# Optimization experiments

Measured on AMD Instinct MI355X. Metric: run time of the kernel, lower is better.

## Reference

```python
import jax, jax.numpy as jnp
import numpy as np

N_NODES = 50000
N_EDGES = 800000
IN_FEATS = 128
H_FEATS = 64
NUM_CLASSES = 2
K = 3
LAMBDA_MAX = 2.0  # standard upper bound for normalized-Laplacian max eigenvalue


def setup_inputs() -> dict:
    key = jax.random.key(0)
    ks = jax.random.split(key, 16)
    s = 0.05
    return {
        "in_feat": jax.random.normal(ks[0], (N_NODES, IN_FEATS), jnp.float32),
        "src": jax.random.randint(ks[1], (N_EDGES,), 0, N_NODES, jnp.int32),
        "dst": jax.random.randint(ks[2], (N_EDGES,), 0, N_NODES, jnp.int32),
        "W1": jax.random.normal(ks[3], (H_FEATS, IN_FEATS), jnp.float32) * s,
        "b1": jnp.zeros((H_FEATS,), jnp.float32),
        "W2": jax.random.normal(ks[4], (H_FEATS, H_FEATS), jnp.float32) * s,
        "b2": jnp.zeros((H_FEATS,), jnp.float32),
        "Wc1": jax.random.normal(ks[5], (H_FEATS, K * H_FEATS), jnp.float32) * s,
        "bc1": jnp.zeros((H_FEATS,), jnp.float32),
        "Wc2": jax.random.normal(ks[6], (H_FEATS, K * H_FEATS), jnp.float32) * s,
        "bc2": jnp.zeros((H_FEATS,), jnp.float32),
        "W3": jax.random.normal(ks[7], (H_FEATS, H_FEATS), jnp.float32) * s,
        "b3": jnp.zeros((H_FEATS,), jnp.float32),
        "W4": jax.random.normal(ks[8], (NUM_CLASSES, H_FEATS), jnp.float32) * s,
        "b4": jnp.zeros((NUM_CLASSES,), jnp.float32),
    }


def _cheb_conv(h, src, dst, d_invsqrt, W, b, k):
    """DGL ChebConv: Chebyshev recursion on scaled normalized Laplacian,
    concat k terms along feature dim, then Linear + relu (default activation)."""
    n = h.shape[0]
    re_norm = 2.0 / LAMBDA_MAX

    def a_norm(x):  # D^{-1/2} A D^{-1/2} x via edge-list SpMM
        msg = (x * d_invsqrt)[src]                              # [E, F]
        agg = jax.ops.segment_sum(msg, dst, num_segments=n)     # [N, F]
        return agg * d_invsqrt

    X0 = h
    Xs = [X0]
    X1 = -re_norm * a_norm(X0) + X0 * (re_norm - 1.0)
    Xs.append(X1)
    for _ in range(2, k):
        Xi = -2.0 * re_norm * a_norm(X1) + X1 * (2.0 * (re_norm - 1.0)) - X0
        Xs.append(Xi)
        X0, X1 = X1, Xi
    Xt = jnp.concatenate(Xs, axis=1)                            # [N, k*F]
    return jax.nn.relu(Xt @ W.T + b)


def reference(in_feat, src, dst, W1, b1, W2, b2, Wc1, bc1, Wc2, bc2, W3, b3, W4, b4):
    n = in_feat.shape[0]
    # in-degrees from dst, clamp(min=1), D^{-1/2}
    deg = jax.ops.segment_sum(jnp.ones_like(dst, jnp.float32), dst, num_segments=n)
    d_invsqrt = jnp.power(jnp.maximum(deg, 1.0), -0.5)[:, None]  # [N, 1]

    h = jax.nn.relu(in_feat @ W1.T + b1)
    h = jax.nn.relu(h @ W2.T + b2)
    h = _cheb_conv(h, src, dst, d_invsqrt, Wc1, bc1, K)
    h = _cheb_conv(h, src, dst, d_invsqrt, Wc2, bc2, K)
    h = jax.nn.relu(h @ W3.T + b3)
    h = h @ W4.T + b4
    return h
```

## Files before the change

kernel.cpp:

```cpp
#include <hip/hip_runtime.h>
#include <hip/hip_fp16.h>
#include <math.h>

#define NN 50000
#define NE 800000
#define INF 128
#define H 64
#define ELLCAP 64
#define NB_G ((NN + 63) / 64)
#define WOFF_W1 0
#define WOFF_W2 8192
#define WOFF_WC1 12288
#define WOFF_WC2 24576
#define WOFF_W3 36864
#define WTOT 40960
#define NB_CVTW (WTOT / 2048)

#define PSHIFT 8
#define NPART2 196
#define CAP 8192
#define NB_BINA 128
#define EPB (NE / NB_BINA)
#define EPT_A 25

#define TSCALE 64.0f
#define TSCALE_INV 0.015625f

typedef _Float16 half8_t __attribute__((ext_vector_type(8)));
typedef float float4_t __attribute__((ext_vector_type(4)));
typedef float float2_t __attribute__((ext_vector_type(2)));

__device__ __forceinline__ half8_t load_cvt8(const float* p) {
  float4 a = *(const float4*)(p);
  float4 b = *(const float4*)(p + 4);
  half8_t h;
  h[0] = (_Float16)a.x; h[1] = (_Float16)a.y; h[2] = (_Float16)a.z; h[3] = (_Float16)a.w;
  h[4] = (_Float16)b.x; h[5] = (_Float16)b.y; h[6] = (_Float16)b.z; h[7] = (_Float16)b.w;
  return h;
}

__device__ __forceinline__ unsigned char enc1(float x) {
  return (unsigned char)(__builtin_amdgcn_cvt_pk_fp8_f32(x, x, 0u, false) & 0xFFu);
}
__device__ __forceinline__ unsigned int enc4(float a, float b, float c, float d) {
  unsigned int v = __builtin_amdgcn_cvt_pk_fp8_f32(a, b, 0u, false);
  v = __builtin_amdgcn_cvt_pk_fp8_f32(c, d, v, true);
  return v;
}
__device__ __forceinline__ void dec8(unsigned int lo, unsigned int hi, float* f) {
  float2_t a = __builtin_amdgcn_cvt_pk_f32_fp8(lo, false);
  float2_t b = __builtin_amdgcn_cvt_pk_f32_fp8(lo, true);
  float2_t c = __builtin_amdgcn_cvt_pk_f32_fp8(hi, false);
  float2_t d = __builtin_amdgcn_cvt_pk_f32_fp8(hi, true);
  f[0] = a[0]; f[1] = a[1]; f[2] = b[0]; f[3] = b[1];
  f[4] = c[0]; f[5] = c[1]; f[6] = d[0]; f[7] = d[1];
}
__device__ __forceinline__ void dec16(uint4 q, float* f) {
  dec8(q.x, q.y, f);
  dec8(q.z, q.w, f + 8);
}

__global__ __launch_bounds__(256) void k_binA(const int* __restrict__ src, const int* __restrict__ dst,
                                              int* __restrict__ gcount, int* __restrict__ bucket,
                                              const float* __restrict__ W1, const float* __restrict__ W2,
                                              const float* __restrict__ Wc1, const float* __restrict__ Wc2,
                                              const float* __restrict__ W3, _Float16* __restrict__ w16) {
  int b = blockIdx.x;
  if (b >= NB_BINA) {
    int i0 = (b - NB_BINA) * 2048 + threadIdx.x * 8;
#pragma unroll
    for (int k = 0; k < 8; ++k) {
      int id = i0 + k;
      if (id < WTOT) {
        float v;
        if (id < WOFF_W2) v = W1[id];
        else if (id < WOFF_WC1) v = W2[id - WOFF_W2];
        else if (id < WOFF_WC2) v = Wc1[id - WOFF_WC1];
        else if (id < WOFF_W3) v = Wc2[id - WOFF_WC2];
        else v = W3[id - WOFF_W3];
        w16[id] = (_Float16)v;
      }
    }
    return;
  }
  __shared__ int s_cnt[NPART2];
  __shared__ int s_base[NPART2];
  const int tid = threadIdx.x;
  if (tid < NPART2) s_cnt[tid] = 0;
  __syncthreads();
  const int e0 = b * EPB;
  int rec[EPT_A];
  int meta[EPT_A];
#pragma unroll
  for (int i = 0; i < EPT_A; ++i) {
    int off = i * 256 + tid;
    meta[i] = -1;
    if (off < EPB) {
      int e = e0 + off;
      int d = __builtin_nontemporal_load(&dst[e]);
      int s = __builtin_nontemporal_load(&src[e]);
      int p = d >> PSHIFT;
      rec[i] = s | ((d & 255) << 16);
      int slot = atomicAdd(&s_cnt[p], 1);
      meta[i] = (p << 13) | slot;
    }
  }
  __syncthreads();
  if (tid < NPART2) s_base[tid] = atomicAdd(&gcount[tid], s_cnt[tid]);
  __syncthreads();
#pragma unroll
  for (int i = 0; i < EPT_A; ++i) {
    if (meta[i] >= 0) {
      int p = meta[i] >> 13;
      int pos = s_base[p] + (meta[i] & 8191);
      if (pos < CAP) bucket[(size_t)p * CAP + pos] = rec[i];
    }
  }
}

__global__ __launch_bounds__(256) void k_binB(const int* __restrict__ gcount, const int* __restrict__ bucket,
                                              unsigned short* __restrict__ ell, int* __restrict__ cnt,
                                              float* __restrict__ dinv32) {
  __shared__ int s_cnt[256];
  const int tid = threadIdx.x;
  const int p = blockIdx.x;
  s_cnt[tid] = 0;
  __syncthreads();
  int n = gcount[p];
  n = n < CAP ? n : CAP;
  const int* bp = bucket + (size_t)p * CAP;
  int j = tid;
  for (; j + 3 * 256 < n; j += 4 * 256) {
    int r0 = bp[j], r1 = bp[j + 256], r2 = bp[j + 512], r3 = bp[j + 768];
    int c0 = atomicAdd(&s_cnt[r0 >> 16], 1);
    int c1 = atomicAdd(&s_cnt[r1 >> 16], 1);
    int c2 = atomicAdd(&s_cnt[r2 >> 16], 1);
    int c3 = atomicAdd(&s_cnt[r3 >> 16], 1);
    if (c0 < ELLCAP) ell[((size_t)((p << PSHIFT) + (r0 >> 16)) << 6) + c0] = (unsigned short)(r0 & 0xFFFF);
    if (c1 < ELLCAP) ell[((size_t)((p << PSHIFT) + (r1 >> 16)) << 6) + c1] = (unsigned short)(r1 & 0xFFFF);
    if (c2 < ELLCAP) ell[((size_t)((p << PSHIFT) + (r2 >> 16)) << 6) + c2] = (unsigned short)(r2 & 0xFFFF);
    if (c3 < ELLCAP) ell[((size_t)((p << PSHIFT) + (r3 >> 16)) << 6) + c3] = (unsigned short)(r3 & 0xFFFF);
  }
  for (; j < n; j += 256) {
    int r = bp[j];
    int dl = r >> 16;
    int c = atomicAdd(&s_cnt[dl], 1);
    if (c < ELLCAP) ell[((size_t)((p << PSHIFT) + dl) << 6) + c] = (unsigned short)(r & 0xFFFF);
  }
  __syncthreads();
  int node = (p << PSHIFT) + tid;
  if (node < NN) {
    int c = s_cnt[tid];
    cnt[node] = c;
    dinv32[node] = 1.0f / sqrtf((float)(c < 1 ? 1 : c));
  }
}

__global__ __launch_bounds__(256) void k_mlp(const float* __restrict__ in_feat,
                                             const _Float16* __restrict__ w16,
                                             const float* __restrict__ b1,
                                             const float* __restrict__ b2,
                                             const float* __restrict__ dinv32,
                                             _Float16* __restrict__ X0c,
                                             unsigned char* __restrict__ X0t, int N) {
  __shared__ _Float16 Hs[64][72];
  const int tid = threadIdx.x;
  const int wave = tid >> 6;
  const int lane = tid & 63;
  const int m = lane & 15;
  const int quad = lane >> 4;
  const int rbase = blockIdx.x * 64 + wave * 16;
  int arow = rbase + m;
  arow = arow < N ? arow : N - 1;
  const float* Ap = in_feat + (size_t)arow * INF + quad * 8;
  const _Float16* B1 = w16 + WOFF_W1 + (size_t)m * INF + quad * 8;
  float4_t acc[4] = {{0.f,0.f,0.f,0.f},{0.f,0.f,0.f,0.f},{0.f,0.f,0.f,0.f},{0.f,0.f,0.f,0.f}};
#pragma unroll
  for (int k0 = 0; k0 < INF; k0 += 32) {
    half8_t a = load_cvt8(Ap + k0);
    half8_t b0 = *(const half8_t*)(B1 + k0);
    half8_t b1f = *(const half8_t*)(B1 + 16 * INF + k0);
    half8_t b2f = *(const half8_t*)(B1 + 32 * INF + k0);
    half8_t b3f = *(const half8_t*)(B1 + 48 * INF + k0);
    acc[0] = __builtin_amdgcn_mfma_f32_16x16x32_f16(a, b0, acc[0], 0, 0, 0);
    acc[1] = __builtin_amdgcn_mfma_f32_16x16x32_f16(a, b1f, acc[1], 0, 0, 0);
    acc[2] = __builtin_amdgcn_mfma_f32_16x16x32_f16(a, b2f, acc[2], 0, 0, 0);
    acc[3] = __builtin_amdgcn_mfma_f32_16x16x32_f16(a, b3f, acc[3], 0, 0, 0);
  }
#pragma unroll
  for (int i = 0; i < 4; ++i)
#pragma unroll
    for (int t = 0; t < 4; ++t)
      Hs[wave * 16 + quad * 4 + i][t * 16 + m] = (_Float16)fmaxf(acc[t][i] + b1[t * 16 + m], 0.f);
  __syncthreads();
  const _Float16* Ap2 = &Hs[wave * 16 + m][quad * 8];
  const _Float16* B2 = w16 + WOFF_W2 + (size_t)m * H + quad * 8;
  float4_t acc2[4] = {{0.f,0.f,0.f,0.f},{0.f,0.f,0.f,0.f},{0.f,0.f,0.f,0.f},{0.f,0.f,0.f,0.f}};
#pragma unroll
  for (int k0 = 0; k0 < H; k0 += 32) {
    half8_t a = *(const half8_t*)(Ap2 + k0);
    half8_t b0 = *(const half8_t*)(B2 + k0);
    half8_t b1f = *(const half8_t*)(B2 + 16 * H + k0);
    half8_t b2f = *(const half8_t*)(B2 + 32 * H + k0);
    half8_t b3f = *(const half8_t*)(B2 + 48 * H + k0);
    acc2[0] = __builtin_amdgcn_mfma_f32_16x16x32_f16(a, b0, acc2[0], 0, 0, 0);
    acc2[1] = __builtin_amdgcn_mfma_f32_16x16x32_f16(a, b1f, acc2[1], 0, 0, 0);
    acc2[2] = __builtin_amdgcn_mfma_f32_16x16x32_f16(a, b2f, acc2[2], 0, 0, 0);
    acc2[3] = __builtin_amdgcn_mfma_f32_16x16x32_f16(a, b3f, acc2[3], 0, 0, 0);
  }
#pragma unroll
  for (int i = 0; i < 4; ++i) {
    int rr = rbase + quad * 4 + i;
    if (rr < N) {
      float dn = TSCALE * dinv32[rr];
#pragma unroll
      for (int t = 0; t < 4; ++t) {
        float v = fmaxf(acc2[t][i] + b2[t * 16 + m], 0.f);
        X0c[((size_t)rr << 6) + t * 16 + m] = (_Float16)v;
        X0t[((size_t)rr << 6) + t * 16 + m] = enc1(dn * v);
      }
    }
  }
}

__global__ __launch_bounds__(256) void k_spmm(const unsigned char* __restrict__ tabs,
                                              _Float16* __restrict__ outc,
                                              unsigned char* __restrict__ outt,
                                              const int* __restrict__ cnt,
                                              const float* __restrict__ dinv32,
                                              const unsigned short* __restrict__ ell, int N) {
  int wv = (blockIdx.x * 256 + threadIdx.x) >> 6;
  int lane = threadIdx.x & 63;
  int node = wv * 8 + (lane >> 3);
  if (node >= N) return;
  int c8 = (lane & 7) * 8;
  int deg0 = cnt[node];
  int deg = deg0 < ELLCAP ? deg0 : ELLCAP;
  const unsigned short* row = ell + ((size_t)node << 6);

  float acc[8] = {0.f, 0.f, 0.f, 0.f, 0.f, 0.f, 0.f, 0.f};
  float f[8];
  int j = 0;
  for (; j + 7 < deg; j += 8) {
    ushort4 ra = *(const ushort4*)(row + j);
    ushort4 rb = *(const ushort4*)(row + j + 4);
    uint2 q0 = *(const uint2*)(tabs + (((size_t)ra.x) << 6) + c8);
    uint2 q1 = *(const uint2*)(tabs + (((size_t)ra.y) << 6) + c8);
    uint2 q2 = *(const uint2*)(tabs + (((size_t)ra.z) << 6) + c8);
    uint2 q3 = *(const uint2*)(tabs + (((size_t)ra.w) << 6) + c8);
    uint2 q4 = *(const uint2*)(tabs + (((size_t)rb.x) << 6) + c8);
    uint2 q5 = *(const uint2*)(tabs + (((size_t)rb.y) << 6) + c8);
    uint2 q6 = *(const uint2*)(tabs + (((size_t)rb.z) << 6) + c8);
    uint2 q7 = *(const uint2*)(tabs + (((size_t)rb.w) << 6) + c8);
    dec8(q0.x, q0.y, f);
#pragma unroll
    for (int k = 0; k < 8; ++k) acc[k] += f[k];
    dec8(q1.x, q1.y, f);
#pragma unroll
    for (int k = 0; k < 8; ++k) acc[k] += f[k];
    dec8(q2.x, q2.y, f);
#pragma unroll
    for (int k = 0; k < 8; ++k) acc[k] += f[k];
    dec8(q3.x, q3.y, f);
#pragma unroll
    for (int k = 0; k < 8; ++k) acc[k] += f[k];
    dec8(q4.x, q4.y, f);
#pragma unroll
    for (int k = 0; k < 8; ++k) acc[k] += f[k];
    dec8(q5.x, q5.y, f);
#pragma unroll
    for (int k = 0; k < 8; ++k) acc[k] += f[k];
    dec8(q6.x, q6.y, f);
#pragma unroll
    for (int k = 0; k < 8; ++k) acc[k] += f[k];
    dec8(q7.x, q7.y, f);
#pragma unroll
    for (int k = 0; k < 8; ++k) acc[k] += f[k];
  }
  for (; j + 3 < deg; j += 4) {
    ushort4 ra = *(const ushort4*)(row + j);
    uint2 q0 = *(const uint2*)(tabs + (((size_t)ra.x) << 6) + c8);
    uint2 q1 = *(const uint2*)(tabs + (((size_t)ra.y) << 6) + c8);
    uint2 q2 = *(const uint2*)(tabs + (((size_t)ra.z) << 6) + c8);
    uint2 q3 = *(const uint2*)(tabs + (((size_t)ra.w) << 6) + c8);
    dec8(q0.x, q0.y, f);
#pragma unroll
    for (int k = 0; k < 8; ++k) acc[k] += f[k];
    dec8(q1.x, q1.y, f);
#pragma unroll
    for (int k = 0; k < 8; ++k) acc[k] += f[k];
    dec8(q2.x, q2.y, f);
#pragma unroll
    for (int k = 0; k < 8; ++k) acc[k] += f[k];
    dec8(q3.x, q3.y, f);
#pragma unroll
    for (int k = 0; k < 8; ++k) acc[k] += f[k];
  }
  for (; j < deg; ++j) {
    size_t s = row[j];
    uint2 q0 = *(const uint2*)(tabs + (s << 6) + c8);
    dec8(q0.x, q0.y, f);
#pragma unroll
    for (int k = 0; k < 8; ++k) acc[k] += f[k];
  }
  float dn = dinv32[node];
  float a = -dn * TSCALE_INV;
  float r[8];
#pragma unroll
  for (int k = 0; k < 8; ++k) r[k] = a * acc[k];
  half8_t ro;
#pragma unroll
  for (int k = 0; k < 8; ++k) ro[k] = (_Float16)r[k];
  *(half8_t*)(outc + ((size_t)node << 6) + c8) = ro;
  float sc = TSCALE * dn;
  uint2 q;
  q.x = enc4(sc * r[0], sc * r[1], sc * r[2], sc * r[3]);
  q.y = enc4(sc * r[4], sc * r[5], sc * r[6], sc * r[7]);
  *(uint2*)(outt + ((size_t)node << 6) + c8) = q;
}

__global__ __launch_bounds__(256) void k_gemmX2(const unsigned char* __restrict__ tabs,
                                                const _Float16* __restrict__ A0,
                                                const _Float16* __restrict__ A1,
                                                const _Float16* __restrict__ B,
                                                const float* __restrict__ bias,
                                                const float* __restrict__ dinv32,
                                                const int* __restrict__ cnt,
                                                const unsigned short* __restrict__ ell,
                                                _Float16* __restrict__ outc,
                                                unsigned char* __restrict__ outt, int N) {
  __shared__ _Float16 X2s[64][72];
  const int tid = threadIdx.x;
  const int wave = tid >> 6;
  const int lane = tid & 63;
  {
    int lrow = wave * 16 + (lane >> 2);
    int gnode = blockIdx.x * 64 + lrow;
    int gc = (lane & 3) * 16;
    float a16[16];
#pragma unroll
    for (int k = 0; k < 16; ++k) a16[k] = 0.f;
    int deg = 0;
    if (gnode < N) {
      int d0 = cnt[gnode];
      deg = d0 < ELLCAP ? d0 : ELLCAP;
    }
    const unsigned short* row = ell + ((size_t)gnode << 6);
    float f[16];
    int j = 0;
    for (; j + 3 < deg; j += 4) {
      ushort4 ra = *(const ushort4*)(row + j);
      uint4 q0 = *(const uint4*)(tabs + (((size_t)ra.x) << 6) + gc);
      uint4 q1 = *(const uint4*)(tabs + (((size_t)ra.y) << 6) + gc);
      uint4 q2 = *(const uint4*)(tabs + (((size_t)ra.z) << 6) + gc);
      uint4 q3 = *(const uint4*)(tabs + (((size_t)ra.w) << 6) + gc);
      dec16(q0, f);
#pragma unroll
      for (int k = 0; k < 16; ++k) a16[k] += f[k];
      dec16(q1, f);
#pragma unroll
      for (int k = 0; k < 16; ++k) a16[k] += f[k];
      dec16(q2, f);
#pragma unroll
      for (int k = 0; k < 16; ++k) a16[k] += f[k];
      dec16(q3, f);
#pragma unroll
      for (int k = 0; k < 16; ++k) a16[k] += f[k];
    }
    for (; j < deg; ++j) {
      size_t s = row[j];
      uint4 q0 = *(const uint4*)(tabs + (s << 6) + gc);
      dec16(q0, f);
#pragma unroll
      for (int k = 0; k < 16; ++k) a16[k] += f[k];
    }
    half8_t o0, o1;
    if (gnode < N) {
      float aa = -2.f * dinv32[gnode] * TSCALE_INV;
      half8_t x0a = *(const half8_t*)(A0 + ((size_t)gnode << 6) + gc);
      half8_t x0b = *(const half8_t*)(A0 + ((size_t)gnode << 6) + gc + 8);
#pragma unroll
      for (int k = 0; k < 8; ++k) {
        o0[k] = (_Float16)(aa * a16[k] - (float)x0a[k]);
        o1[k] = (_Float16)(aa * a16[k + 8] - (float)x0b[k]);
      }
    } else {
#pragma unroll
      for (int k = 0; k < 8; ++k) { o0[k] = (_Float16)0.f; o1[k] = (_Float16)0.f; }
    }
    *(half8_t*)(&X2s[lrow][gc]) = o0;
    *(half8_t*)(&X2s[lrow][gc + 8]) = o1;
  }
  __syncthreads();
  const int m = lane & 15;
  const int quad = lane >> 4;
  const int rbase = blockIdx.x * 64 + wave * 16;
  int arow = rbase + m;
  arow = arow < N ? arow : N - 1;
  const size_t ro = ((size_t)arow << 6) + quad * 8;
  const _Float16* Bp = B + (size_t)m * 192 + quad * 8;
  float4_t acc[4] = {{0.f,0.f,0.f,0.f},{0.f,0.f,0.f,0.f},{0.f,0.f,0.f,0.f},{0.f,0.f,0.f,0.f}};
#pragma unroll
  for (int k0 = 0; k0 < 192; k0 += 32) {
    half8_t a;
    if (k0 < 64) a = *(const half8_t*)(A0 + ro + k0);
    else if (k0 < 128) a = *(const half8_t*)(A1 + ro + (k0 - 64));
    else a = *(const half8_t*)(&X2s[wave * 16 + m][quad * 8 + (k0 - 128)]);
    half8_t b0 = *(const half8_t*)(Bp + k0);
    half8_t b1f = *(const half8_t*)(Bp + 16 * 192 + k0);
    half8_t b2f = *(const half8_t*)(Bp + 32 * 192 + k0);
    half8_t b3f = *(const half8_t*)(Bp + 48 * 192 + k0);
    acc[0] = __builtin_amdgcn_mfma_f32_16x16x32_f16(a, b0, acc[0], 0, 0, 0);
    acc[1] = __builtin_amdgcn_mfma_f32_16x16x32_f16(a, b1f, acc[1], 0, 0, 0);
    acc[2] = __builtin_amdgcn_mfma_f32_16x16x32_f16(a, b2f, acc[2], 0, 0, 0);
    acc[3] = __builtin_amdgcn_mfma_f32_16x16x32_f16(a, b3f, acc[3], 0, 0, 0);
  }
#pragma unroll
  for (int i = 0; i < 4; ++i) {
    int rr = rbase + quad * 4 + i;
    if (rr < N) {
      float dn = TSCALE * dinv32[rr];
#pragma unroll
      for (int t = 0; t < 4; ++t) {
        float v = fmaxf(acc[t][i] + bias[t * 16 + m], 0.f);
        outc[((size_t)rr << 6) + t * 16 + m] = (_Float16)v;
        outt[((size_t)rr << 6) + t * 16 + m] = enc1(dn * v);
      }
    }
  }
}

__global__ __launch_bounds__(256) void k_tail2(const unsigned char* __restrict__ tabs,
                                               const _Float16* __restrict__ A0,
                                               const _Float16* __restrict__ A1,
                                               const _Float16* __restrict__ w16,
                                               const float* __restrict__ bc2,
                                               const float* __restrict__ b3,
                                               const float* __restrict__ W4,
                                               const float* __restrict__ b4,
                                               const float* __restrict__ dinv32,
                                               const int* __restrict__ cnt,
                                               const unsigned short* __restrict__ ell,
                                               float* __restrict__ out, int N) {
  __shared__ _Float16 Y2s[64][72];
  __shared__ _Float16 Hs2[64][72];
  __shared__ float Hs3[64][65];
  const int tid = threadIdx.x;
  const int wave = tid >> 6;
  const int lane = tid & 63;
  {
    int lrow = wave * 16 + (lane >> 2);
    int gnode = blockIdx.x * 64 + lrow;
    int gc = (lane & 3) * 16;
    float a16[16];
#pragma unroll
    for (int k = 0; k < 16; ++k) a16[k] = 0.f;
    int deg = 0;
    if (gnode < N) {
      int d0 = cnt[gnode];
      deg = d0 < ELLCAP ? d0 : ELLCAP;
    }
    const unsigned short* row = ell + ((size_t)gnode << 6);
    float f[16];
    int j = 0;
    for (; j + 3 < deg; j += 4) {
      ushort4 ra = *(const ushort4*)(row + j);
      uint4 q0 = *(const uint4*)(tabs + (((size_t)ra.x) << 6) + gc);
      uint4 q1 = *(const uint4*)(tabs + (((size_t)ra.y) << 6) + gc);
      uint4 q2 = *(const uint4*)(tabs + (((size_t)ra.z) << 6) + gc);
      uint4 q3 = *(const uint4*)(tabs + (((size_t)ra.w) << 6) + gc);
      dec16(q0, f);
#pragma unroll
      for (int k = 0; k < 16; ++k) a16[k] += f[k];
      dec16(q1, f);
#pragma unroll
      for (int k = 0; k < 16; ++k) a16[k] += f[k];
      dec16(q2, f);
#pragma unroll
      for (int k = 0; k < 16; ++k) a16[k] += f[k];
      dec16(q3, f);
#pragma unroll
      for (int k = 0; k < 16; ++k) a16[k] += f[k];
    }
    for (; j < deg; ++j) {
      size_t s = row[j];
      uint4 q0 = *(const uint4*)(tabs + (s << 6) + gc);
      dec16(q0, f);
#pragma unroll
      for (int k = 0; k < 16; ++k) a16[k] += f[k];
    }
    half8_t o0, o1;
    if (gnode < N) {
      float aa = -2.f * dinv32[gnode] * TSCALE_INV;
      half8_t y0a = *(const half8_t*)(A0 + ((size_t)gnode << 6) + gc);
      half8_t y0b = *(const half8_t*)(A0 + ((size_t)gnode << 6) + gc + 8);
#pragma unroll
      for (int k = 0; k < 8; ++k) {
        o0[k] = (_Float16)(aa * a16[k] - (float)y0a[k]);
        o1[k] = (_Float16)(aa * a16[k + 8] - (float)y0b[k]);
      }
    } else {
#pragma unroll
      for (int k = 0; k < 8; ++k) { o0[k] = (_Float16)0.f; o1[k] = (_Float16)0.f; }
    }
    *(half8_t*)(&Y2s[lrow][gc]) = o0;
    *(half8_t*)(&Y2s[lrow][gc + 8]) = o1;
  }
  __syncthreads();
  const int m = lane & 15;
  const int quad = lane >> 4;
  const int rbase = blockIdx.x * 64 + wave * 16;
  int arow = rbase + m;
  arow = arow < N ? arow : N - 1;
  {
    const size_t ro = ((size_t)arow << 6) + quad * 8;
    const _Float16* Bp = w16 + WOFF_WC2 + (size_t)m * 192 + quad * 8;
    float4_t acc[4] = {{0.f,0.f,0.f,0.f},{0.f,0.f,0.f,0.f},{0.f,0.f,0.f,0.f},{0.f,0.f,0.f,0.f}};
#pragma unroll
    for (int k0 = 0; k0 < 192; k0 += 32) {
      half8_t a;
      if (k0 < 64) a = *(const half8_t*)(A0 + ro + k0);
      else if (k0 < 128) a = *(const half8_t*)(A1 + ro + (k0 - 64));
      else a = *(const half8_t*)(&Y2s[wave * 16 + m][quad * 8 + (k0 - 128)]);
      half8_t b0 = *(const half8_t*)(Bp + k0);
      half8_t b1f = *(const half8_t*)(Bp + 16 * 192 + k0);
      half8_t b2f = *(const half8_t*)(Bp + 32 * 192 + k0);
      half8_t b3f = *(const half8_t*)(Bp + 48 * 192 + k0);
      acc[0] = __builtin_amdgcn_mfma_f32_16x16x32_f16(a, b0, acc[0], 0, 0, 0);
      acc[1] = __builtin_amdgcn_mfma_f32_16x16x32_f16(a, b1f, acc[1], 0, 0, 0);
      acc[2] = __builtin_amdgcn_mfma_f32_16x16x32_f16(a, b2f, acc[2], 0, 0, 0);
      acc[3] = __builtin_amdgcn_mfma_f32_16x16x32_f16(a, b3f, acc[3], 0, 0, 0);
    }
#pragma unroll
    for (int i = 0; i < 4; ++i)
#pragma unroll
      for (int t = 0; t < 4; ++t)
        Hs2[wave * 16 + quad * 4 + i][t * 16 + m] =
            (_Float16)fmaxf(acc[t][i] + bc2[t * 16 + m], 0.f);
  }
  __syncthreads();
  {
    const _Float16* Ap = &Hs2[wave * 16 + m][quad * 8];
    const _Float16* Bp = w16 + WOFF_W3 + (size_t)m * H + quad * 8;
    float4_t acc[4] = {{0.f,0.f,0.f,0.f},{0.f,0.f,0.f,0.f},{0.f,0.f,0.f,0.f},{0.f,0.f,0.f,0.f}};
#pragma unroll
    for (int k0 = 0; k0 < H; k0 += 32) {
      half8_t a = *(const half8_t*)(Ap + k0);
      half8_t b0 = *(const half8_t*)(Bp + k0);
      half8_t b1f = *(const half8_t*)(Bp + 16 * H + k0);
      half8_t b2f = *(const half8_t*)(Bp + 32 * H + k0);
      half8_t b3f = *(const half8_t*)(Bp + 48 * H + k0);
      acc[0] = __builtin_amdgcn_mfma_f32_16x16x32_f16(a, b0, acc[0], 0, 0, 0);
      acc[1] = __builtin_amdgcn_mfma_f32_16x16x32_f16(a, b1f, acc[1], 0, 0, 0);
      acc[2] = __builtin_amdgcn_mfma_f32_16x16x32_f16(a, b2f, acc[2], 0, 0, 0);
      acc[3] = __builtin_amdgcn_mfma_f32_16x16x32_f16(a, b3f, acc[3], 0, 0, 0);
    }
#pragma unroll
    for (int i = 0; i < 4; ++i)
#pragma unroll
      for (int t = 0; t < 4; ++t)
        Hs3[wave * 16 + quad * 4 + i][t * 16 + m] = fmaxf(acc[t][i] + b3[t * 16 + m], 0.f);
  }
  __syncthreads();
  if (tid < 128) {
    int r = tid >> 1;
    int c = tid & 1;
    int row = blockIdx.x * 64 + r;
    if (row < N) {
      const float* w4 = W4 + c * 64;
      float s = 0.f;
#pragma unroll
      for (int k = 0; k < 64; ++k) s = fmaf(Hs3[r][k], w4[k], s);
      out[(size_t)row * 2 + c] = s + b4[c];
    }
  }
}

extern "C" void kernel_launch(void* const* d_in, const int* in_sizes, int n_in,
                              void* d_out, int out_size, void* d_ws, size_t ws_size,
                              hipStream_t stream) {
  const float* in_feat = (const float*)d_in[0];
  const int* src = (const int*)d_in[1];
  const int* dst = (const int*)d_in[2];
  const float* W1 = (const float*)d_in[3];
  const float* b1 = (const float*)d_in[4];
  const float* W2 = (const float*)d_in[5];
  const float* b2 = (const float*)d_in[6];
  const float* Wc1 = (const float*)d_in[7];
  const float* bc1 = (const float*)d_in[8];
  const float* Wc2 = (const float*)d_in[9];
  const float* bc2 = (const float*)d_in[10];
  const float* W3 = (const float*)d_in[11];
  const float* b3 = (const float*)d_in[12];
  const float* W4 = (const float*)d_in[13];
  const float* b4 = (const float*)d_in[14];
  float* out = (float*)d_out;

  char* ws = (char*)d_ws;
  size_t o = 0;
  auto carve = [&](size_t bytes) -> void* {
    o = (o + 255) & ~(size_t)255;
    void* p = ws + o;
    o += bytes;
    return p;
  };
  int* cnt = (int*)carve((size_t)NN * 4);
  unsigned short* ell = (unsigned short*)carve((size_t)NN * ELLCAP * 2);
  float* dinv32 = (float*)carve((size_t)NN * 4);
  _Float16* w16 = (_Float16*)carve((size_t)WTOT * 2);
  _Float16* X0c = (_Float16*)carve((size_t)NN * H * 2);
  unsigned char* X0t = (unsigned char*)carve((size_t)NN * H);
  _Float16* X1c = (_Float16*)carve((size_t)NN * H * 2);
  unsigned char* X1t = (unsigned char*)carve((size_t)NN * H);
  _Float16* Y0c = (_Float16*)carve((size_t)NN * H * 2);
  unsigned char* Y0t = (unsigned char*)carve((size_t)NN * H);
  _Float16* Y1c = (_Float16*)carve((size_t)NN * H * 2);
  unsigned char* Y1t = (unsigned char*)carve((size_t)NN * H);
  int* gcount = (int*)carve((size_t)NPART2 * 4);
  int* bucket = (int*)Y0c;
  (void)ws_size; (void)in_sizes; (void)n_in; (void)out_size;

  const int NB_S = (NN + 31) / 32;

  hipMemsetAsync(gcount, 0, (size_t)NPART2 * 4, stream);
  k_binA<<<NB_BINA + NB_CVTW, 256, 0, stream>>>(src, dst, gcount, bucket, W1, W2, Wc1, Wc2, W3, w16);
  k_binB<<<NPART2, 256, 0, stream>>>(gcount, bucket, ell, cnt, dinv32);
  k_mlp<<<NB_G, 256, 0, stream>>>(in_feat, w16, b1, b2, dinv32, X0c, X0t, NN);
  k_spmm<<<NB_S, 256, 0, stream>>>(X0t, X1c, X1t, cnt, dinv32, ell, NN);
  k_gemmX2<<<NB_G, 256, 0, stream>>>(X1t, X0c, X1c, w16 + WOFF_WC1, bc1, dinv32, cnt, ell, Y0c, Y0t, NN);
  k_spmm<<<NB_S, 256, 0, stream>>>(Y0t, Y1c, Y1t, cnt, dinv32, ell, NN);
  k_tail2<<<NB_G, 256, 0, stream>>>(Y1t, Y0c, Y1c, w16, bc2, b3, W4, b4, dinv32, cnt, ell, out, NN);
}
```

Baseline: 225.9 us.

## Sort nodes by degree within 64-node groups and stage ELL rows in LDS

k_binB now builds each partition's ELL rows in shared memory, then writes them to global memory as contiguous row copies instead of scattered 2-byte stores. It also computes a per-64-node counting sort by degree (perm8). The SpMM and fused gemm kernels use perm8 so that lanes in a wave handle nodes with similar degree, which is meant to reduce divergence in the neighbor loops. This costs an extra indirection load per node, about 35KB of extra LDS in binB, and full 128-byte row writes even for low-degree nodes.

```diff
diff --git a/kernel.cpp b/kernel.cpp
--- a/kernel.cpp
+++ b/kernel.cpp
@@ -18,6 +18,7 @@
 
 #define PSHIFT 8
 #define NPART2 196
+#define NPERM (NPART2 * 256)
 #define CAP 8192
 #define NB_BINA 128
 #define EPB (NE / NB_BINA)
@@ -120,11 +121,17 @@
 
 __global__ __launch_bounds__(256) void k_binB(const int* __restrict__ gcount, const int* __restrict__ bucket,
                                               unsigned short* __restrict__ ell, int* __restrict__ cnt,
-                                              float* __restrict__ dinv32) {
+                                              float* __restrict__ dinv32,
+                                              unsigned char* __restrict__ perm8) {
+  __shared__ unsigned short s_ell[256][68];
   __shared__ int s_cnt[256];
+  __shared__ int s_hist[4][65];
+  __shared__ int s_off[4][65];
+  __shared__ int s_base[4][65];
   const int tid = threadIdx.x;
   const int p = blockIdx.x;
   s_cnt[tid] = 0;
+  for (int i = tid; i < 4 * 65; i += 256) { ((int*)s_hist)[i] = 0; ((int*)s_off)[i] = 0; }
   __syncthreads();
   int n = gcount[p];
   n = n < CAP ? n : CAP;
@@ -136,23 +143,41 @@
     int c1 = atomicAdd(&s_cnt[r1 >> 16], 1);
     int c2 = atomicAdd(&s_cnt[r2 >> 16], 1);
     int c3 = atomicAdd(&s_cnt[r3 >> 16], 1);
-    if (c0 < ELLCAP) ell[((size_t)((p << PSHIFT) + (r0 >> 16)) << 6) + c0] = (unsigned short)(r0 & 0xFFFF);
-    if (c1 < ELLCAP) ell[((size_t)((p << PSHIFT) + (r1 >> 16)) << 6) + c1] = (unsigned short)(r1 & 0xFFFF);
-    if (c2 < ELLCAP) ell[((size_t)((p << PSHIFT) + (r2 >> 16)) << 6) + c2] = (unsigned short)(r2 & 0xFFFF);
-    if (c3 < ELLCAP) ell[((size_t)((p << PSHIFT) + (r3 >> 16)) << 6) + c3] = (unsigned short)(r3 & 0xFFFF);
+    if (c0 < ELLCAP) s_ell[r0 >> 16][c0] = (unsigned short)(r0 & 0xFFFF);
+    if (c1 < ELLCAP) s_ell[r1 >> 16][c1] = (unsigned short)(r1 & 0xFFFF);
+    if (c2 < ELLCAP) s_ell[r2 >> 16][c2] = (unsigned short)(r2 & 0xFFFF);
+    if (c3 < ELLCAP) s_ell[r3 >> 16][c3] = (unsigned short)(r3 & 0xFFFF);
   }
   for (; j < n; j += 256) {
     int r = bp[j];
     int dl = r >> 16;
     int c = atomicAdd(&s_cnt[dl], 1);
-    if (c < ELLCAP) ell[((size_t)((p << PSHIFT) + dl) << 6) + c] = (unsigned short)(r & 0xFFFF);
+    if (c < ELLCAP) s_ell[dl][c] = (unsigned short)(r & 0xFFFF);
   }
   __syncthreads();
   int node = (p << PSHIFT) + tid;
+  int deg = 0;
   if (node < NN) {
     int c = s_cnt[tid];
     cnt[node] = c;
     dinv32[node] = 1.0f / sqrtf((float)(c < 1 ? 1 : c));
+    deg = c < ELLCAP ? c : ELLCAP;
+  }
+  int g = tid >> 6;
+  atomicAdd(&s_hist[g][deg], 1);
+  __syncthreads();
+  if (tid < 4) {
+    int acc = 0;
+    for (int k = 0; k <= 64; ++k) { s_base[tid][k] = acc; acc += s_hist[tid][k]; }
+  }
+  __syncthreads();
+  int pos = s_base[g][deg] + atomicAdd(&s_off[g][deg], 1);
+  perm8[(size_t)(p << PSHIFT) + (g << 6) + pos] = (unsigned char)(tid & 63);
+  if (node < NN) {
+    const uint2* srcv = (const uint2*)&s_ell[tid][0];
+    uint2* dstv = (uint2*)(ell + ((size_t)node << 6));
+#pragma unroll
+    for (int k = 0; k < 16; ++k) dstv[k] = srcv[k];
   }
 }
 
@@ -228,10 +253,13 @@
                                               unsigned char* __restrict__ outt,
                                               const int* __restrict__ cnt,
                                               const float* __restrict__ dinv32,
-                                              const unsigned short* __restrict__ ell, int N) {
+                                              const unsigned short* __restrict__ ell,
+                                              const unsigned char* __restrict__ perm8, int N) {
   int wv = (blockIdx.x * 256 + threadIdx.x) >> 6;
   int lane = threadIdx.x & 63;
-  int node = wv * 8 + (lane >> 3);
+  int slot = wv * 8 + (lane >> 3);
+  if (slot >= NPERM) return;
+  int node = (slot & ~63) + perm8[slot];
   if (node >= N) return;
   int c8 = (lane & 7) * 8;
   int deg0 = cnt[node];
@@ -327,6 +355,7 @@
                                                 const float* __restrict__ dinv32,
                                                 const int* __restrict__ cnt,
                                                 const unsigned short* __restrict__ ell,
+                                                const unsigned char* __restrict__ perm8,
                                                 _Float16* __restrict__ outc,
                                                 unsigned char* __restrict__ outt, int N) {
   __shared__ _Float16 X2s[64][72];
@@ -334,7 +363,8 @@
   const int wave = tid >> 6;
   const int lane = tid & 63;
   {
-    int lrow = wave * 16 + (lane >> 2);
+    int lslot = wave * 16 + (lane >> 2);
+    int lrow = perm8[(size_t)blockIdx.x * 64 + lslot];
     int gnode = blockIdx.x * 64 + lrow;
     int gc = (lane & 3) * 16;
     float a16[16];
@@ -441,6 +471,7 @@
                                                const float* __restrict__ dinv32,
                                                const int* __restrict__ cnt,
                                                const unsigned short* __restrict__ ell,
+                                               const unsigned char* __restrict__ perm8,
                                                float* __restrict__ out, int N) {
   __shared__ _Float16 Y2s[64][72];
   __shared__ _Float16 Hs2[64][72];
@@ -449,7 +480,8 @@
   const int wave = tid >> 6;
   const int lane = tid & 63;
   {
-    int lrow = wave * 16 + (lane >> 2);
+    int lslot = wave * 16 + (lane >> 2);
+    int lrow = perm8[(size_t)blockIdx.x * 64 + lslot];
     int gnode = blockIdx.x * 64 + lrow;
     int gc = (lane & 3) * 16;
     float a16[16];
@@ -608,6 +640,7 @@
   unsigned short* ell = (unsigned short*)carve((size_t)NN * ELLCAP * 2);
   float* dinv32 = (float*)carve((size_t)NN * 4);
   _Float16* w16 = (_Float16*)carve((size_t)WTOT * 2);
+  unsigned char* perm8 = (unsigned char*)carve((size_t)NPERM);
   _Float16* X0c = (_Float16*)carve((size_t)NN * H * 2);
   unsigned char* X0t = (unsigned char*)carve((size_t)NN * H);
   _Float16* X1c = (_Float16*)carve((size_t)NN * H * 2);
@@ -620,14 +653,14 @@
   int* bucket = (int*)Y0c;
   (void)ws_size; (void)in_sizes; (void)n_in; (void)out_size;
 
-  const int NB_S = (NN + 31) / 32;
+  const int NB_S = NPERM / 32;
 
   hipMemsetAsync(gcount, 0, (size_t)NPART2 * 4, stream);
   k_binA<<<NB_BINA + NB_CVTW, 256, 0, stream>>>(src, dst, gcount, bucket, W1, W2, Wc1, Wc2, W3, w16);
-  k_binB<<<NPART2, 256, 0, stream>>>(gcount, bucket, ell, cnt, dinv32);
+  k_binB<<<NPART2, 256, 0, stream>>>(gcount, bucket, ell, cnt, dinv32, perm8);
   k_mlp<<<NB_G, 256, 0, stream>>>(in_feat, w16, b1, b2, dinv32, X0c, X0t, NN);
-  k_spmm<<<NB_S, 256, 0, stream>>>(X0t, X1c, X1t, cnt, dinv32, ell, NN);
-  k_gemmX2<<<NB_G, 256, 0, stream>>>(X1t, X0c, X1c, w16 + WOFF_WC1, bc1, dinv32, cnt, ell, Y0c, Y0t, NN);
-  k_spmm<<<NB_S, 256, 0, stream>>>(Y0t, Y1c, Y1t, cnt, dinv32, ell, NN);
-  k_tail2<<<NB_G, 256, 0, stream>>>(Y1t, Y0c, Y1c, w16, bc2, b3, W4, b4, dinv32, cnt, ell, out, NN);
-}
+  k_spmm<<<NB_S, 256, 0, stream>>>(X0t, X1c, X1t, cnt, dinv32, ell, perm8, NN);
+  k_gemmX2<<<NB_G, 256, 0, stream>>>(X1t, X0c, X1c, w16 + WOFF_WC1, bc1, dinv32, cnt, ell, perm8, Y0c, Y0t, NN);
+  k_spmm<<<NB_S, 256, 0, stream>>>(Y0t, Y1c, Y1t, cnt, dinv32, ell, perm8, NN);
+  k_tail2<<<NB_G, 256, 0, stream>>>(Y1t, Y0c, Y1c, w16, bc2, b3, W4, b4, dinv32, cnt, ell, perm8, out, NN);
+}
```

New measurement: 226.9 us. No clear change (+0.4%).

## Run MLP alongside edge binning and stage ELL rows in shared memory

Applied to the files above, without the earlier changes.

The first MLP blocks now run in the same launch as the edge-binning blocks, since the MLP no longer needs degree information. The fp8 degree-scaled copy of X0 is now produced in binB, after degrees are known, by re-reading the fp16 X0. binB builds ELL rows in shared memory and writes each node's row out as contiguous vector stores, replacing scattered 2-byte global stores. The counter memset is folded into the weight-conversion kernel. This costs an extra read of X0c and about 35KB of LDS per binB block.

```diff
diff --git a/kernel.cpp b/kernel.cpp
--- a/kernel.cpp
+++ b/kernel.cpp
@@ -60,67 +60,137 @@
   dec8(q.z, q.w, f + 8);
 }
 
-__global__ __launch_bounds__(256) void k_binA(const int* __restrict__ src, const int* __restrict__ dst,
-                                              int* __restrict__ gcount, int* __restrict__ bucket,
-                                              const float* __restrict__ W1, const float* __restrict__ W2,
-                                              const float* __restrict__ Wc1, const float* __restrict__ Wc2,
-                                              const float* __restrict__ W3, _Float16* __restrict__ w16) {
+__global__ __launch_bounds__(256) void k_pre(const float* __restrict__ W1, const float* __restrict__ W2,
+                                             const float* __restrict__ Wc1, const float* __restrict__ Wc2,
+                                             const float* __restrict__ W3, _Float16* __restrict__ w16,
+                                             int* __restrict__ gcount) {
   int b = blockIdx.x;
-  if (b >= NB_BINA) {
-    int i0 = (b - NB_BINA) * 2048 + threadIdx.x * 8;
-#pragma unroll
-    for (int k = 0; k < 8; ++k) {
-      int id = i0 + k;
-      if (id < WTOT) {
-        float v;
-        if (id < WOFF_W2) v = W1[id];
-        else if (id < WOFF_WC1) v = W2[id - WOFF_W2];
-        else if (id < WOFF_WC2) v = Wc1[id - WOFF_WC1];
-        else if (id < WOFF_W3) v = Wc2[id - WOFF_WC2];
-        else v = W3[id - WOFF_W3];
-        w16[id] = (_Float16)v;
+  if (b == NB_CVTW) {
+    if (threadIdx.x < NPART2) gcount[threadIdx.x] = 0;
+    return;
+  }
+  int i0 = b * 2048 + threadIdx.x * 8;
+#pragma unroll
+  for (int k = 0; k < 8; ++k) {
+    int id = i0 + k;
+    if (id < WTOT) {
+      float v;
+      if (id < WOFF_W2) v = W1[id];
+      else if (id < WOFF_WC1) v = W2[id - WOFF_W2];
+      else if (id < WOFF_WC2) v = Wc1[id - WOFF_WC1];
+      else if (id < WOFF_W3) v = Wc2[id - WOFF_WC2];
+      else v = W3[id - WOFF_W3];
+      w16[id] = (_Float16)v;
+    }
+  }
+}
+
+__global__ __launch_bounds__(256) void k_binA_mlp(const int* __restrict__ src, const int* __restrict__ dst,
+                                                  int* __restrict__ gcount, int* __restrict__ bucket,
+                                                  const float* __restrict__ in_feat,
+                                                  const _Float16* __restrict__ w16,
+                                                  const float* __restrict__ b1,
+                                                  const float* __restrict__ b2,
+                                                  _Float16* __restrict__ X0c, int N) {
+  __shared__ int s_shared[NPART2 * 2];
+  const int tid = threadIdx.x;
+  int b = blockIdx.x;
+  if (b < NB_BINA) {
+    int* s_cnt = s_shared;
+    int* s_base = s_shared + NPART2;
+    if (tid < NPART2) s_cnt[tid] = 0;
+    __syncthreads();
+    const int e0 = b * EPB;
+    int rec[EPT_A];
+    int meta[EPT_A];
+#pragma unroll
+    for (int i = 0; i < EPT_A; ++i) {
+      int off = i * 256 + tid;
+      meta[i] = -1;
+      if (off < EPB) {
+        int e = e0 + off;
+        int d = __builtin_nontemporal_load(&dst[e]);
+        int s = __builtin_nontemporal_load(&src[e]);
+        int p = d >> PSHIFT;
+        rec[i] = s | ((d & 255) << 16);
+        int slot = atomicAdd(&s_cnt[p], 1);
+        meta[i] = (p << 13) | slot;
       }
     }
+    __syncthreads();
+    if (tid < NPART2) s_base[tid] = atomicAdd(&gcount[tid], s_cnt[tid]);
+    __syncthreads();
+#pragma unroll
+    for (int i = 0; i < EPT_A; ++i) {
+      if (meta[i] >= 0) {
+        int p = meta[i] >> 13;
+        int pos = s_base[p] + (meta[i] & 8191);
+        if (pos < CAP) bucket[(size_t)p * CAP + pos] = rec[i];
+      }
+    }
     return;
   }
-  __shared__ int s_cnt[NPART2];
-  __shared__ int s_base[NPART2];
-  const int tid = threadIdx.x;
-  if (tid < NPART2) s_cnt[tid] = 0;
+  __shared__ _Float16 Hs[64][72];
+  const int wave = tid >> 6;
+  const int lane = tid & 63;
+  const int m = lane & 15;
+  const int quad = lane >> 4;
+  const int rbase = (b - NB_BINA) * 64 + wave * 16;
+  int arow = rbase + m;
+  arow = arow < N ? arow : N - 1;
+  const float* Ap = in_feat + (size_t)arow * INF + quad * 8;
+  const _Float16* B1 = w16 + WOFF_W1 + (size_t)m * INF + quad * 8;
+  float4_t acc[4] = {{0.f,0.f,0.f,0.f},{0.f,0.f,0.f,0.f},{0.f,0.f,0.f,0.f},{0.f,0.f,0.f,0.f}};
+#pragma unroll
+  for (int k0 = 0; k0 < INF; k0 += 32) {
+    half8_t a = load_cvt8(Ap + k0);
+    half8_t b0 = *(const half8_t*)(B1 + k0);
+    half8_t b1f = *(const half8_t*)(B1 + 16 * INF + k0);
+    half8_t b2f = *(const half8_t*)(B1 + 32 * INF + k0);
+    half8_t b3f = *(const half8_t*)(B1 + 48 * INF + k0);
+    acc[0] = __builtin_amdgcn_mfma_f32_16x16x32_f16(a, b0, acc[0], 0, 0, 0);
+    acc[1] = __builtin_amdgcn_mfma_f32_16x16x32_f16(a, b1f, acc[1], 0, 0, 0);
+    acc[2] = __builtin_amdgcn_mfma_f32_16x16x32_f16(a, b2f, acc[2], 0, 0, 0);
+    acc[3] = __builtin_amdgcn_mfma_f32_16x16x32_f16(a, b3f, acc[3], 0, 0, 0);
+  }
+#pragma unroll
+  for (int i = 0; i < 4; ++i)
+#pragma unroll
+    for (int t = 0; t < 4; ++t)
+      Hs[wave * 16 + quad * 4 + i][t * 16 + m] = (_Float16)fmaxf(acc[t][i] + b1[t * 16 + m], 0.f);
   __syncthreads();
-  const int e0 = b * EPB;
-  int rec[EPT_A];
-  int meta[EPT_A];
-#pragma unroll
-  for (int i = 0; i < EPT_A; ++i) {
-    int off = i * 256 + tid;
-    meta[i] = -1;
-    if (off < EPB) {
-      int e = e0 + off;
-      int d = __builtin_nontemporal_load(&dst[e]);
-      int s = __builtin_nontemporal_load(&src[e]);
-      int p = d >> PSHIFT;
-      rec[i] = s | ((d & 255) << 16);
-      int slot = atomicAdd(&s_cnt[p], 1);
-      meta[i] = (p << 13) | slot;
-    }
-  }
-  __syncthreads();
-  if (tid < NPART2) s_base[tid] = atomicAdd(&gcount[tid], s_cnt[tid]);
-  __syncthreads();
-#pragma unroll
-  for (int i = 0; i < EPT_A; ++i) {
-    if (meta[i] >= 0) {
-      int p = meta[i] >> 13;
-      int pos = s_base[p] + (meta[i] & 8191);
-      if (pos < CAP) bucket[(size_t)p * CAP + pos] = rec[i];
+  const _Float16* Ap2 = &Hs[wave * 16 + m][quad * 8];
+  const _Float16* B2 = w16 + WOFF_W2 + (size_t)m * H + quad * 8;
+  float4_t acc2[4] = {{0.f,0.f,0.f,0.f},{0.f,0.f,0.f,0.f},{0.f,0.f,0.f,0.f},{0.f,0.f,0.f,0.f}};
+#pragma unroll
+  for (int k0 = 0; k0 < H; k0 += 32) {
+    half8_t a = *(const half8_t*)(Ap2 + k0);
+    half8_t b0 = *(const half8_t*)(B2 + k0);
+    half8_t b1f = *(const half8_t*)(B2 + 16 * H + k0);
+    half8_t b2f = *(const half8_t*)(B2 + 32 * H + k0);
+    half8_t b3f = *(const half8_t*)(B2 + 48 * H + k0);
+    acc2[0] = __builtin_amdgcn_mfma_f32_16x16x32_f16(a, b0, acc2[0], 0, 0, 0);
+    acc2[1] = __builtin_amdgcn_mfma_f32_16x16x32_f16(a, b1f, acc2[1], 0, 0, 0);
+    acc2[2] = __builtin_amdgcn_mfma_f32_16x16x32_f16(a, b2f, acc2[2], 0, 0, 0);
+    acc2[3] = __builtin_amdgcn_mfma_f32_16x16x32_f16(a, b3f, acc2[3], 0, 0, 0);
+  }
+#pragma unroll
+  for (int i = 0; i < 4; ++i) {
+    int rr = rbase + quad * 4 + i;
+    if (rr < N) {
+#pragma unroll
+      for (int t = 0; t < 4; ++t)
+        X0c[((size_t)rr << 6) + t * 16 + m] = (_Float16)fmaxf(acc2[t][i] + b2[t * 16 + m], 0.f);
     }
   }
 }
 
 __global__ __launch_bounds__(256) void k_binB(const int* __restrict__ gcount, const int* __restrict__ bucket,
                                               unsigned short* __restrict__ ell, int* __restrict__ cnt,
-                                              float* __restrict__ dinv32) {
+                                              float* __restrict__ dinv32,
+                                              const _Float16* __restrict__ X0c,
+                                              unsigned char* __restrict__ X0t) {
+  __shared__ unsigned short s_ell[256][68];
   __shared__ int s_cnt[256];
   const int tid = threadIdx.x;
   const int p = blockIdx.x;
@@ -136,89 +206,41 @@
     int c1 = atomicAdd(&s_cnt[r1 >> 16], 1);
     int c2 = atomicAdd(&s_cnt[r2 >> 16], 1);
     int c3 = atomicAdd(&s_cnt[r3 >> 16], 1);
-    if (c0 < ELLCAP) ell[((size_t)((p << PSHIFT) + (r0 >> 16)) << 6) + c0] = (unsigned short)(r0 & 0xFFFF);
-    if (c1 < ELLCAP) ell[((size_t)((p << PSHIFT) + (r1 >> 16)) << 6) + c1] = (unsigned short)(r1 & 0xFFFF);
-    if (c2 < ELLCAP) ell[((size_t)((p << PSHIFT) + (r2 >> 16)) << 6) + c2] = (unsigned short)(r2 & 0xFFFF);
-    if (c3 < ELLCAP) ell[((size_t)((p << PSHIFT) + (r3 >> 16)) << 6) + c3] = (unsigned short)(r3 & 0xFFFF);
+    if (c0 < ELLCAP) s_ell[r0 >> 16][c0] = (unsigned short)(r0 & 0xFFFF);
+    if (c1 < ELLCAP) s_ell[r1 >> 16][c1] = (unsigned short)(r1 & 0xFFFF);
+    if (c2 < ELLCAP) s_ell[r2 >> 16][c2] = (unsigned short)(r2 & 0xFFFF);
+    if (c3 < ELLCAP) s_ell[r3 >> 16][c3] = (unsigned short)(r3 & 0xFFFF);
   }
   for (; j < n; j += 256) {
     int r = bp[j];
     int dl = r >> 16;
     int c = atomicAdd(&s_cnt[dl], 1);
-    if (c < ELLCAP) ell[((size_t)((p << PSHIFT) + dl) << 6) + c] = (unsigned short)(r & 0xFFFF);
+    if (c < ELLCAP) s_ell[dl][c] = (unsigned short)(r & 0xFFFF);
   }
   __syncthreads();
   int node = (p << PSHIFT) + tid;
   if (node < NN) {
     int c = s_cnt[tid];
     cnt[node] = c;
-    dinv32[node] = 1.0f / sqrtf((float)(c < 1 ? 1 : c));
-  }
-}
-
-__global__ __launch_bounds__(256) void k_mlp(const float* __restrict__ in_feat,
-                                             const _Float16* __restrict__ w16,
-                                             const float* __restrict__ b1,
-                                             const float* __restrict__ b2,
-                                             const float* __restrict__ dinv32,
-                                             _Float16* __restrict__ X0c,
-                                             unsigned char* __restrict__ X0t, int N) {
-  __shared__ _Float16 Hs[64][72];
-  const int tid = threadIdx.x;
-  const int wave = tid >> 6;
-  const int lane = tid & 63;
-  const int m = lane & 15;
-  const int quad = lane >> 4;
-  const int rbase = blockIdx.x * 64 + wave * 16;
-  int arow = rbase + m;
-  arow = arow < N ? arow : N - 1;
-  const float* Ap = in_feat + (size_t)arow * INF + quad * 8;
-  const _Float16* B1 = w16 + WOFF_W1 + (size_t)m * INF + quad * 8;
-  float4_t acc[4] = {{0.f,0.f,0.f,0.f},{0.f,0.f,0.f,0.f},{0.f,0.f,0.f,0.f},{0.f,0.f,0.f,0.f}};
-#pragma unroll
-  for (int k0 = 0; k0 < INF; k0 += 32) {
-    half8_t a = load_cvt8(Ap + k0);
-    half8_t b0 = *(const half8_t*)(B1 + k0);
-    half8_t b1f = *(const half8_t*)(B1 + 16 * INF + k0);
-    half8_t b2f = *(const half8_t*)(B1 + 32 * INF + k0);
-    half8_t b3f = *(const half8_t*)(B1 + 48 * INF + k0);
-    acc[0] = __builtin_amdgcn_mfma_f32_16x16x32_f16(a, b0, acc[0], 0, 0, 0);
-    acc[1] = __builtin_amdgcn_mfma_f32_16x16x32_f16(a, b1f, acc[1], 0, 0, 0);
-    acc[2] = __builtin_amdgcn_mfma_f32_16x16x32_f16(a, b2f, acc[2], 0, 0, 0);
-    acc[3] = __builtin_amdgcn_mfma_f32_16x16x32_f16(a, b3f, acc[3], 0, 0, 0);
-  }
-#pragma unroll
-  for (int i = 0; i < 4; ++i)
-#pragma unroll
-    for (int t = 0; t < 4; ++t)
-      Hs[wave * 16 + quad * 4 + i][t * 16 + m] = (_Float16)fmaxf(acc[t][i] + b1[t * 16 + m], 0.f);
-  __syncthreads();
-  const _Float16* Ap2 = &Hs[wave * 16 + m][quad * 8];
-  const _Float16* B2 = w16 + WOFF_W2 + (size_t)m * H + quad * 8;
-  float4_t acc2[4] = {{0.f,0.f,0.f,0.f},{0.f,0.f,0.f,0.f},{0.f,0.f,0.f,0.f},{0.f,0.f,0.f,0.f}};
-#pragma unroll
-  for (int k0 = 0; k0 < H; k0 += 32) {
-    half8_t a = *(const half8_t*)(Ap2 + k0);
-    half8_t b0 = *(const half8_t*)(B2 + k0);
-    half8_t b1f = *(const half8_t*)(B2 + 16 * H + k0);
-    half8_t b2f = *(const half8_t*)(B2 + 32 * H + k0);
-    half8_t b3f = *(const half8_t*)(B2 + 48 * H + k0);
-    acc2[0] = __builtin_amdgcn_mfma_f32_16x16x32_f16(a, b0, acc2[0], 0, 0, 0);
-    acc2[1] = __builtin_amdgcn_mfma_f32_16x16x32_f16(a, b1f, acc2[1], 0, 0, 0);
-    acc2[2] = __builtin_amdgcn_mfma_f32_16x16x32_f16(a, b2f, acc2[2], 0, 0, 0);
-    acc2[3] = __builtin_amdgcn_mfma_f32_16x16x32_f16(a, b3f, acc2[3], 0, 0, 0);
-  }
-#pragma unroll
-  for (int i = 0; i < 4; ++i) {
-    int rr = rbase + quad * 4 + i;
-    if (rr < N) {
-      float dn = TSCALE * dinv32[rr];
-#pragma unroll
-      for (int t = 0; t < 4; ++t) {
-        float v = fmaxf(acc2[t][i] + b2[t * 16 + m], 0.f);
-        X0c[((size_t)rr << 6) + t * 16 + m] = (_Float16)v;
-        X0t[((size_t)rr << 6) + t * 16 + m] = enc1(dn * v);
-      }
+    float dinv = 1.0f / sqrtf((float)(c < 1 ? 1 : c));
+    dinv32[node] = dinv;
+    const uint2* srcv = (const uint2*)&s_ell[tid][0];
+    uint2* dstv = (uint2*)(ell + ((size_t)node << 6));
+#pragma unroll
+    for (int k = 0; k < 16; ++k) dstv[k] = srcv[k];
+    float dn = TSCALE * dinv;
+    const half8_t* xr = (const half8_t*)(X0c + ((size_t)node << 6));
+    uint4* qo = (uint4*)(X0t + ((size_t)node << 6));
+#pragma unroll
+    for (int g = 0; g < 4; ++g) {
+      half8_t h0 = xr[2 * g];
+      half8_t h1 = xr[2 * g + 1];
+      uint4 q;
+      q.x = enc4(dn * (float)h0[0], dn * (float)h0[1], dn * (float)h0[2], dn * (float)h0[3]);
+      q.y = enc4(dn * (float)h0[4], dn * (float)h0[5], dn * (float)h0[6], dn * (float)h0[7]);
+      q.z = enc4(dn * (float)h1[0], dn * (float)h1[1], dn * (float)h1[2], dn * (float)h1[3]);
+      q.w = enc4(dn * (float)h1[4], dn * (float)h1[5], dn * (float)h1[6], dn * (float)h1[7]);
+      qo[g] = q;
     }
   }
 }
@@ -622,10 +644,9 @@
 
   const int NB_S = (NN + 31) / 32;
 
-  hipMemsetAsync(gcount, 0, (size_t)NPART2 * 4, stream);
-  k_binA<<<NB_BINA + NB_CVTW, 256, 0, stream>>>(src, dst, gcount, bucket, W1, W2, Wc1, Wc2, W3, w16);
-  k_binB<<<NPART2, 256, 0, stream>>>(gcount, bucket, ell, cnt, dinv32);
-  k_mlp<<<NB_G, 256, 0, stream>>>(in_feat, w16, b1, b2, dinv32, X0c, X0t, NN);
+  k_pre<<<NB_CVTW + 1, 256, 0, stream>>>(W1, W2, Wc1, Wc2, W3, w16, gcount);
+  k_binA_mlp<<<NB_BINA + NB_G, 256, 0, stream>>>(src, dst, gcount, bucket, in_feat, w16, b1, b2, X0c, NN);
+  k_binB<<<NPART2, 256, 0, stream>>>(gcount, bucket, ell, cnt, dinv32, X0c, X0t);
   k_spmm<<<NB_S, 256, 0, stream>>>(X0t, X1c, X1t, cnt, dinv32, ell, NN);
   k_gemmX2<<<NB_G, 256, 0, stream>>>(X1t, X0c, X1c, w16 + WOFF_WC1, bc1, dinv32, cnt, ell, Y0c, Y0t, NN);
   k_spmm<<<NB_S, 256, 0, stream>>>(Y0t, Y1c, Y1t, cnt, dinv32, ell, NN);
```

Measured after the change: 219.5 us. -2.9%, faster.
